# Kernel optimization log

Hardware: AMD Instinct MI355X
Metric: run time of the kernel (lower is better)

The kernel has to match this reference:

```python
import jax, jax.numpy as jnp
import numpy as np

H = 16
D = 1024
HD = D // H

def setup_inputs() -> dict:
    key = jax.random.key(0)
    ks = jax.random.split(key, 5)
    x = jax.random.normal(ks[0], (2, 2048, D), dtype=jnp.float32)
    w_qkv = jax.random.normal(ks[1], (D, 3 * D), dtype=jnp.float32) / np.sqrt(D)
    b_qkv = jax.random.normal(ks[2], (3 * D,), dtype=jnp.float32) * 0.01
    w_o = jax.random.normal(ks[3], (D, D), dtype=jnp.float32) / np.sqrt(D)
    b_o = jax.random.normal(ks[4], (D,), dtype=jnp.float32) * 0.01
    return {"x": x, "w_qkv": w_qkv, "b_qkv": b_qkv, "w_o": w_o, "b_o": b_o}

def reference(x, w_qkv, b_qkv, w_o, b_o):
    b, s, d = x.shape
    qkv = x @ w_qkv + b_qkv                      # [b, s, 3d]
    q, k, v = jnp.split(qkv, 3, axis=-1)
    q = q.reshape(b, s, H, HD)
    k = k.reshape(b, s, H, HD)
    v = v.reshape(b, s, H, HD)
    scores = jnp.einsum('bqhd,bkhd->bhqk', q, k) / jnp.sqrt(jnp.float32(HD))
    attn = jax.nn.softmax(scores, axis=-1)       # [b, h, s, s]
    out = jnp.einsum('bhqk,bkhd->bqhd', attn, v).reshape(b, s, d)
    return out @ w_o + b_o
```

## Files before the change

### kernel.cpp

```cpp
#include <hip/hip_runtime.h>
#include <hip/hip_bf16.h>

typedef unsigned int u32;
typedef unsigned short u16;
typedef __attribute__((ext_vector_type(8))) short bf16x8;
typedef __attribute__((ext_vector_type(4))) float f32x4;
typedef __attribute__((ext_vector_type(16))) float f32x16;
typedef __attribute__((ext_vector_type(8))) u16 u16x8;
typedef __attribute__((ext_vector_type(2))) u32 u32x2;
typedef __attribute__((ext_vector_type(4))) u32 u32x4;

#define MFMA32(A, B, C) __builtin_amdgcn_mfma_f32_32x32x16_bf16(A, B, C, 0, 0, 0)

#define C_SCALE 0.1803368801111244f

__device__ __forceinline__ u16 f2bf(float f) {
  __hip_bfloat16 h = __float2bfloat16(f);
  u16 u;
  __builtin_memcpy(&u, &h, 2);
  return u;
}

__device__ __forceinline__ u32 pk2(float a, float b) {
  return (u32)f2bf(a) | ((u32)f2bf(b) << 16);
}

__device__ __forceinline__ float exp2fast(float x) {
#if __has_builtin(__builtin_amdgcn_exp2f)
  return __builtin_amdgcn_exp2f(x);
#else
  return exp2f(x);
#endif
}

__device__ __forceinline__ u32x2 pl32swap(u32 a, u32 b) {
  return __builtin_amdgcn_permlane32_swap(a, b, false, false);
}

__device__ __forceinline__ void g2l16(const void* g, void* l) {
  __builtin_amdgcn_global_load_lds(
      (const __attribute__((address_space(1))) u32*)g,
      (__attribute__((address_space(3))) u32*)l, 16, 0, 0);
}

__device__ __forceinline__ void wtrans_tile(const float* __restrict__ in,
                                            u16* __restrict__ out, int R, int C,
                                            int scale_n, float scale,
                                            int c0, int r0, float (*t)[33]) {
  const int tr = threadIdx.x >> 3, tc = (threadIdx.x & 7) << 2;
  const float4 v = *(const float4*)(in + (size_t)(r0 + tr) * C + c0 + tc);
  t[tr][tc] = v.x; t[tr][tc + 1] = v.y; t[tr][tc + 2] = v.z; t[tr][tc + 3] = v.w;
  __syncthreads();
  const float s = (c0 + tr < scale_n) ? scale : 1.f;
  u32 p0 = pk2(t[tc][tr] * s, t[tc + 1][tr] * s);
  u32 p1 = pk2(t[tc + 2][tr] * s, t[tc + 3][tr] * s);
  u32* dst = (u32*)(out + (size_t)(c0 + tr) * R + r0 + tc);
  dst[0] = p0;
  dst[1] = p1;
}

__global__ __launch_bounds__(256) void prep(
    const float* __restrict__ x, u16* __restrict__ xb,
    const float* __restrict__ w_qkv, u16* __restrict__ wqkvt,
    const float* __restrict__ w_o, u16* __restrict__ wot) {
  __shared__ float t[32][33];
  const int bx = blockIdx.x;
  if (bx < 2048) {
    const int i = bx * 256 + threadIdx.x;
    const float4* p = (const float4*)x + (size_t)i * 2;
    const float4 a = p[0], b = p[1];
    u16x8 o;
    o[0] = f2bf(a.x); o[1] = f2bf(a.y); o[2] = f2bf(a.z); o[3] = f2bf(a.w);
    o[4] = f2bf(b.x); o[5] = f2bf(b.y); o[6] = f2bf(b.z); o[7] = f2bf(b.w);
    *((u16x8*)xb + i) = o;
  } else if (bx < 5120) {
    const int tb = bx - 2048;
    wtrans_tile(w_qkv, wqkvt, 1024, 3072, 1024, C_SCALE,
                (tb % 96) << 5, (tb / 96) << 5, t);
  } else {
    const int tb = bx - 5120;
    wtrans_tile(w_o, wot, 1024, 1024, 0, 1.f,
                (tb % 32) << 5, (tb / 32) << 5, t);
  }
}

template <int BN, int OUT_BF16>
__global__ __launch_bounds__(256) void gemm_mfma(
    const u16* __restrict__ A, const u16* __restrict__ Bt,
    const float* __restrict__ bias, void* __restrict__ Cv, int N, int K,
    int bsn, float bsc) {
  constexpr int NI = BN / 64;
  __shared__ u16 As[2][128 * 32];
  __shared__ u16 Bs[2][BN * 32];
  const int tid = threadIdx.x;
  const int l = tid & 63;
  const int lq = l & 31, hw = l >> 5;
  const int w = tid >> 6;
  const int wm = (w >> 1) << 6, wn = (w & 1) * (BN / 2);

  const int nx = gridDim.x;
  const int flat = blockIdx.y * nx + blockIdx.x;
  const int cpx = (nx * gridDim.y) >> 3;
  const int swz = (flat & 7) * cpx + (flat >> 3);
  const int bm = (swz / nx) << 7, bn = (swz % nx) * BN;

  f32x16 acc[2][NI];
  const f32x16 z16 = {};
#pragma unroll
  for (int i = 0; i < 2; ++i)
#pragma unroll
    for (int j = 0; j < NI; ++j) acc[i][j] = z16;

  const int bi0 = tid, bi1 = 256 + tid;
  const int r0 = bi0 >> 2, lb0 = (bi0 & 3) ^ ((r0 >> 1) & 3);
  const int r1 = bi1 >> 2, lb1 = (bi1 & 3) ^ ((r1 >> 1) & 3);
  const u16* a0 = A + (size_t)(bm + r0) * K + lb0 * 8;
  const u16* a1 = A + (size_t)(bm + r1) * K + lb1 * 8;
  const u16* b0 = Bt + (size_t)(bn + r0) * K + lb0 * 8;
  const u16* b1 = Bt + (size_t)(bn + r1) * K + lb1 * 8;

  for (int k0 = 0; k0 < K; k0 += 64) {
    __syncthreads();
    g2l16(a0 + k0, (char*)As[0] + bi0 * 16);
    g2l16(a1 + k0, (char*)As[0] + bi1 * 16);
    g2l16(b0 + k0, (char*)Bs[0] + bi0 * 16);
    if constexpr (BN == 128) g2l16(b1 + k0, (char*)Bs[0] + bi1 * 16);
    g2l16(a0 + k0 + 32, (char*)As[1] + bi0 * 16);
    g2l16(a1 + k0 + 32, (char*)As[1] + bi1 * 16);
    g2l16(b0 + k0 + 32, (char*)Bs[1] + bi0 * 16);
    if constexpr (BN == 128) g2l16(b1 + k0 + 32, (char*)Bs[1] + bi1 * 16);
    __syncthreads();
#pragma unroll
    for (int sub = 0; sub < 2; ++sub) {
#pragma unroll
      for (int ks = 0; ks < 2; ++ks) {
        bf16x8 af[2], bfv[NI];
#pragma unroll
        for (int mi = 0; mi < 2; ++mi) {
          const int row = wm + mi * 32 + lq;
          const int phys = (ks * 2 + hw) ^ ((row >> 1) & 3);
          af[mi] = *(const bf16x8*)((const char*)As[sub] + row * 64 + (phys << 4));
        }
#pragma unroll
        for (int ni = 0; ni < NI; ++ni) {
          const int row = wn + ni * 32 + lq;
          const int phys = (ks * 2 + hw) ^ ((row >> 1) & 3);
          bfv[ni] = *(const bf16x8*)((const char*)Bs[sub] + row * 64 + (phys << 4));
        }
#pragma unroll
        for (int mi = 0; mi < 2; ++mi)
#pragma unroll
          for (int ni = 0; ni < NI; ++ni)
            acc[mi][ni] = MFMA32(af[mi], bfv[ni], acc[mi][ni]);
      }
    }
  }

  float bv[NI];
#pragma unroll
  for (int ni = 0; ni < NI; ++ni) {
    const int col = bn + wn + ni * 32 + lq;
    bv[ni] = bias[col] * (col < bsn ? bsc : 1.f);
  }
  if (OUT_BF16) {
    u16* C = (u16*)Cv;
#pragma unroll
    for (int mi = 0; mi < 2; ++mi)
#pragma unroll
      for (int ni = 0; ni < NI; ++ni)
#pragma unroll
        for (int r = 0; r < 16; ++r) {
          const int row = bm + wm + mi * 32 + (r & 3) + 8 * (r >> 2) + 4 * hw;
          const int col = bn + wn + ni * 32 + lq;
          C[(size_t)row * N + col] = f2bf(acc[mi][ni][r] + bv[ni]);
        }
  } else {
    float* C = (float*)Cv;
#pragma unroll
    for (int mi = 0; mi < 2; ++mi)
#pragma unroll
      for (int ni = 0; ni < NI; ++ni)
#pragma unroll
        for (int r = 0; r < 16; ++r) {
          const int row = bm + wm + mi * 32 + (r & 3) + 8 * (r >> 2) + 4 * hw;
          const int col = bn + wn + ni * 32 + lq;
          C[(size_t)row * N + col] = acc[mi][ni][r] + bv[ni];
        }
  }
}

__global__ __launch_bounds__(256) void vtrans(const u16* __restrict__ qkvb,
                                              u16* __restrict__ vt) {
  const int wid = (blockIdx.x << 2) + (threadIdx.x >> 6);
  const int l = threadIdx.x & 63;
  const int dc = wid & 7, st = (wid >> 3) & 31, h = (wid >> 8) & 15, b = wid >> 12;
  const int s = (st << 6) + l;
  const u16x8 v = *(const u16x8*)(qkvb + (size_t)(b * 2048 + s) * 3072 + 2048 + h * 64 + dc * 8);
  u16* dst = vt + ((size_t)(((b << 4) + h) << 6) + (dc << 3)) * 2048 + s;
#pragma unroll
  for (int j = 0; j < 8; ++j) dst[(size_t)j * 2048] = v[j];
}

__global__ __launch_bounds__(256, 2) void attn_mfma(
    const u16* __restrict__ qkvb, const u16* __restrict__ vt,
    u16* __restrict__ attnb) {
  __shared__ u16 Ks2[2][64 * 64];
  __shared__ u16 Vs2[2][64 * 64];

  const int flat = (blockIdx.z << 8) + (blockIdx.y << 4) + blockIdx.x;
  const int swz = (flat & 7) * 64 + (flat >> 3);
  const int qt = swz & 15, head = (swz >> 4) & 15, b = swz >> 8;

  const int tid = threadIdx.x, w = tid >> 6, l = tid & 63;
  const int lq = l & 31, hw = l >> 5;
  const size_t sb = (size_t)b * 2048;
  const f32x16 z16 = {};

  const int bi0 = tid, bi1 = 256 + tid;
  const int sr0 = bi0 >> 3, slb0 = (bi0 & 7) ^ (sr0 & 7);
  const int sr1 = bi1 >> 3, slb1 = (bi1 & 7) ^ (sr1 & 7);

  const u16* kbase = qkvb + sb * 3072 + 1024 + head * 64;
  const u16* vbase = vt + ((size_t)((b << 4) + head) << 6) * 2048;

  const u16* kp0 = kbase + (size_t)sr0 * 3072 + slb0 * 8;
  const u16* kp1 = kbase + (size_t)sr1 * 3072 + slb1 * 8;
  const u16* vp0 = vbase + (size_t)sr0 * 2048 + slb0 * 8;
  const u16* vp1 = vbase + (size_t)sr1 * 2048 + slb1 * 8;

  bf16x8 qf[4];
  {
    const u16* qr = qkvb + (sb + (size_t)qt * 128 + (w << 5) + lq) * 3072 +
                    head * 64 + hw * 8;
#pragma unroll
    for (int dc = 0; dc < 4; ++dc) qf[dc] = *(const bf16x8*)(qr + dc * 16);
  }

  const short one_bf = (short)0x3F80;
  const bf16x8 ones = {one_bf, one_bf, one_bf, one_bf,
                       one_bf, one_bf, one_bf, one_bf};

  f32x16 o0 = z16, o1 = z16, l_acc = z16;
  const int xsw = lq & 7;

  for (int kt = 0; kt < 16; ++kt) {
    const size_t ko = (size_t)kt << 7;
    __syncthreads();
    g2l16(kp0 + ko * 3072, (char*)Ks2[0] + bi0 * 16);
    g2l16(kp1 + ko * 3072, (char*)Ks2[0] + bi1 * 16);
    g2l16(kp0 + (ko + 64) * 3072, (char*)Ks2[1] + bi0 * 16);
    g2l16(kp1 + (ko + 64) * 3072, (char*)Ks2[1] + bi1 * 16);
    g2l16(vp0 + ko, (char*)Vs2[0] + bi0 * 16);
    g2l16(vp1 + ko, (char*)Vs2[0] + bi1 * 16);
    g2l16(vp0 + ko + 64, (char*)Vs2[1] + bi0 * 16);
    g2l16(vp1 + ko + 64, (char*)Vs2[1] + bi1 * 16);
    __syncthreads();

    const char* K0 = (const char*)Ks2[0];
    const char* K1 = (const char*)Ks2[1];
    const char* V0 = (const char*)Vs2[0];
    const char* V1 = (const char*)Vs2[1];

    f32x16 s00 = z16, s01 = z16, s10 = z16, s11 = z16;
#pragma unroll
    for (int dc = 0; dc < 4; ++dc) {
      const int off = (((2 * dc + hw) ^ xsw) << 4);
      s00 = MFMA32(*(const bf16x8*)(K0 + lq * 128 + off), qf[dc], s00);
      s01 = MFMA32(*(const bf16x8*)(K0 + (32 + lq) * 128 + off), qf[dc], s01);
      s10 = MFMA32(*(const bf16x8*)(K1 + lq * 128 + off), qf[dc], s10);
      s11 = MFMA32(*(const bf16x8*)(K1 + (32 + lq) * 128 + off), qf[dc], s11);
    }

    bf16x8 pa[4];
#pragma unroll
    for (int kc = 0; kc < 4; ++kc) {
      const f32x16 s = (kc < 2) ? s00 : s01;
      const int q0 = (kc & 1) * 8;
      const u32 W01 = pk2(exp2fast(s[q0 + 0]), exp2fast(s[q0 + 1]));
      const u32 W23 = pk2(exp2fast(s[q0 + 2]), exp2fast(s[q0 + 3]));
      const u32 W45 = pk2(exp2fast(s[q0 + 4]), exp2fast(s[q0 + 5]));
      const u32 W67 = pk2(exp2fast(s[q0 + 6]), exp2fast(s[q0 + 7]));
      const u32x2 rA = pl32swap(W01, W45);
      const u32x2 rB = pl32swap(W23, W67);
      const u32x4 wds = {rA.x, rB.x, rA.y, rB.y};
      pa[kc] = __builtin_bit_cast(bf16x8, wds);
    }
#pragma unroll
    for (int kc = 0; kc < 4; ++kc) {
      const int off = (((2 * kc + hw) ^ xsw) << 4);
      l_acc = MFMA32(pa[kc], ones, l_acc);
      o0 = MFMA32(pa[kc], *(const bf16x8*)(V0 + lq * 128 + off), o0);
      o1 = MFMA32(pa[kc], *(const bf16x8*)(V0 + (32 + lq) * 128 + off), o1);
    }

    bf16x8 pb[4];
#pragma unroll
    for (int kc = 0; kc < 4; ++kc) {
      const f32x16 s = (kc < 2) ? s10 : s11;
      const int q0 = (kc & 1) * 8;
      const u32 W01 = pk2(exp2fast(s[q0 + 0]), exp2fast(s[q0 + 1]));
      const u32 W23 = pk2(exp2fast(s[q0 + 2]), exp2fast(s[q0 + 3]));
      const u32 W45 = pk2(exp2fast(s[q0 + 4]), exp2fast(s[q0 + 5]));
      const u32 W67 = pk2(exp2fast(s[q0 + 6]), exp2fast(s[q0 + 7]));
      const u32x2 rA = pl32swap(W01, W45);
      const u32x2 rB = pl32swap(W23, W67);
      const u32x4 wds = {rA.x, rB.x, rA.y, rB.y};
      pb[kc] = __builtin_bit_cast(bf16x8, wds);
    }
#pragma unroll
    for (int kc = 0; kc < 4; ++kc) {
      const int off = (((2 * kc + hw) ^ xsw) << 4);
      l_acc = MFMA32(pb[kc], ones, l_acc);
      o0 = MFMA32(pb[kc], *(const bf16x8*)(V1 + lq * 128 + off), o0);
      o1 = MFMA32(pb[kc], *(const bf16x8*)(V1 + (32 + lq) * 128 + off), o1);
    }
  }

  u16* ob = attnb + (sb + (size_t)qt * 128 + (w << 5)) * 1024 + head * 64;
#pragma unroll
  for (int r = 0; r < 16; ++r) {
    const int qo = (r & 3) + 8 * (r >> 2) + 4 * hw;
    const float iv = 1.f / l_acc[r];
    ob[(size_t)qo * 1024 + lq] = f2bf(o0[r] * iv);
    ob[(size_t)qo * 1024 + 32 + lq] = f2bf(o1[r] * iv);
  }
}

extern "C" void kernel_launch(void* const* d_in, const int* in_sizes, int n_in,
                              void* d_out, int out_size, void* d_ws, size_t ws_size,
                              hipStream_t stream) {
  const float* x     = (const float*)d_in[0];
  const float* w_qkv = (const float*)d_in[1];
  const float* b_qkv = (const float*)d_in[2];
  const float* w_o   = (const float*)d_in[3];
  const float* b_o   = (const float*)d_in[4];
  float* out = (float*)d_out;

  u16* xb    = (u16*)d_ws;
  u16* wqkvt = xb + (size_t)4096 * 1024;
  u16* wot   = wqkvt + (size_t)3072 * 1024;
  u16* qkvb  = wot + (size_t)1024 * 1024;
  u16* vtb   = qkvb + (size_t)4096 * 3072;
  u16* attnb = vtb + (size_t)2 * 16 * 64 * 2048;

  prep<<<dim3(6144), dim3(256), 0, stream>>>(x, xb, w_qkv, wqkvt, w_o, wot);

  gemm_mfma<128, 1><<<dim3(24, 32), dim3(256), 0, stream>>>(
      xb, wqkvt, b_qkv, qkvb, 3072, 1024, 1024, C_SCALE);

  vtrans<<<dim3(2048), dim3(256), 0, stream>>>(qkvb, vtb);
  attn_mfma<<<dim3(16, 16, 2), dim3(256), 0, stream>>>(qkvb, vtb, attnb);

  gemm_mfma<64, 0><<<dim3(16, 32), dim3(256), 0, stream>>>(
      attnb, wot, b_o, out, 1024, 1024, 0, 1.f);
}
```

Measured before the change: 118.4 us.

## Prefetch next K/V tile into registers during attention compute

After: 119.7 us. About the same (+1.1%).

```diff
diff --git a/kernel.cpp b/kernel.cpp
--- a/kernel.cpp
+++ b/kernel.cpp
@@ -243,18 +243,37 @@
   f32x16 o0 = z16, o1 = z16, l_acc = z16;
   const int xsw = lq & 7;
 
+  u32x4 kr[4], vr[4];
+  kr[0] = *(const u32x4*)(kp0);
+  kr[1] = *(const u32x4*)(kp1);
+  kr[2] = *(const u32x4*)(kp0 + (size_t)64 * 3072);
+  kr[3] = *(const u32x4*)(kp1 + (size_t)64 * 3072);
+  vr[0] = *(const u32x4*)(vp0);
+  vr[1] = *(const u32x4*)(vp1);
+  vr[2] = *(const u32x4*)(vp0 + 64);
+  vr[3] = *(const u32x4*)(vp1 + 64);
+  *(u32x4*)((char*)Ks2[0] + bi0 * 16) = kr[0];
+  *(u32x4*)((char*)Ks2[0] + bi1 * 16) = kr[1];
+  *(u32x4*)((char*)Ks2[1] + bi0 * 16) = kr[2];
+  *(u32x4*)((char*)Ks2[1] + bi1 * 16) = kr[3];
+  *(u32x4*)((char*)Vs2[0] + bi0 * 16) = vr[0];
+  *(u32x4*)((char*)Vs2[0] + bi1 * 16) = vr[1];
+  *(u32x4*)((char*)Vs2[1] + bi0 * 16) = vr[2];
+  *(u32x4*)((char*)Vs2[1] + bi1 * 16) = vr[3];
+  __syncthreads();
+
   for (int kt = 0; kt < 16; ++kt) {
-    const size_t ko = (size_t)kt << 7;
-    __syncthreads();
-    g2l16(kp0 + ko * 3072, (char*)Ks2[0] + bi0 * 16);
-    g2l16(kp1 + ko * 3072, (char*)Ks2[0] + bi1 * 16);
-    g2l16(kp0 + (ko + 64) * 3072, (char*)Ks2[1] + bi0 * 16);
-    g2l16(kp1 + (ko + 64) * 3072, (char*)Ks2[1] + bi1 * 16);
-    g2l16(vp0 + ko, (char*)Vs2[0] + bi0 * 16);
-    g2l16(vp1 + ko, (char*)Vs2[0] + bi1 * 16);
-    g2l16(vp0 + ko + 64, (char*)Vs2[1] + bi0 * 16);
-    g2l16(vp1 + ko + 64, (char*)Vs2[1] + bi1 * 16);
-    __syncthreads();
+    if (kt < 15) {
+      const size_t ko = (size_t)(kt + 1) << 7;
+      kr[0] = *(const u32x4*)(kp0 + ko * 3072);
+      kr[1] = *(const u32x4*)(kp1 + ko * 3072);
+      kr[2] = *(const u32x4*)(kp0 + (ko + 64) * 3072);
+      kr[3] = *(const u32x4*)(kp1 + (ko + 64) * 3072);
+      vr[0] = *(const u32x4*)(vp0 + ko);
+      vr[1] = *(const u32x4*)(vp1 + ko);
+      vr[2] = *(const u32x4*)(vp0 + ko + 64);
+      vr[3] = *(const u32x4*)(vp1 + ko + 64);
+    }
 
     const char* K0 = (const char*)Ks2[0];
     const char* K1 = (const char*)Ks2[1];
@@ -314,6 +333,19 @@
       o0 = MFMA32(pb[kc], *(const bf16x8*)(V1 + lq * 128 + off), o0);
       o1 = MFMA32(pb[kc], *(const bf16x8*)(V1 + (32 + lq) * 128 + off), o1);
     }
+
+    __syncthreads();
+    if (kt < 15) {
+      *(u32x4*)((char*)Ks2[0] + bi0 * 16) = kr[0];
+      *(u32x4*)((char*)Ks2[0] + bi1 * 16) = kr[1];
+      *(u32x4*)((char*)Ks2[1] + bi0 * 16) = kr[2];
+      *(u32x4*)((char*)Ks2[1] + bi1 * 16) = kr[3];
+      *(u32x4*)((char*)Vs2[0] + bi0 * 16) = vr[0];
+      *(u32x4*)((char*)Vs2[0] + bi1 * 16) = vr[1];
+      *(u32x4*)((char*)Vs2[1] + bi0 * 16) = vr[2];
+      *(u32x4*)((char*)Vs2[1] + bi1 * 16) = vr[3];
+    }
+    __syncthreads();
   }
 
   u16* ob = attnb + (sb + (size_t)qt * 128 + (w << 5)) * 1024 + head * 64;
```
